# Performance work log

Measured on AMD Instinct MI355X. Metric: run time of the kernel, lower is better.

## Reference

```python
import jax, jax.numpy as jnp
import numpy as np

N = 100000   # vertices
T = 128      # temporal depth
E = 1600000  # edges (avg degree 16)
K = 9        # conv kernel size
PAD = 4      # 'same' padding -> T preserved
L = 3        # number of layers


def setup_inputs() -> dict:
    key = jax.random.key(0)
    ks = jax.random.split(key, 6)
    x = jax.random.normal(ks[0], (N, T), dtype=jnp.float32)
    edge_index = jax.random.randint(ks[1], (2, E), 0, N, dtype=jnp.int32)
    conv_w = jax.random.normal(ks[2], (L, 1, 1, K), dtype=jnp.float32) * (1.0 / np.sqrt(K))
    conv_b = jax.random.normal(ks[3], (L, 1), dtype=jnp.float32) * 0.1
    W_out = jax.random.normal(ks[4], (3, N), dtype=jnp.float32) * (1.0 / np.sqrt(N))
    b_out = jax.random.normal(ks[5], (3,), dtype=jnp.float32) * 0.1
    return {"x": x, "edge_index": edge_index, "conv_w": conv_w,
            "conv_b": conv_b, "W_out": W_out, "b_out": b_out}


def _conv1d(x, w, b):
    # x: [N, T], w: [1, 1, K] (OIH), b: [1]; torch Conv1d = cross-correlation.
    y = jax.lax.conv_general_dilated(
        x[:, None, :], w, window_strides=(1,), padding=[(PAD, PAD)],
        dimension_numbers=("NCH", "OIH", "NCH"))
    return y[:, 0, :] + b  # [N, T]


def reference(x, edge_index, conv_w, conv_b, W_out, b_out):
    # add_self_loops: append (i, i) for every node
    loop = jnp.arange(N, dtype=edge_index.dtype)
    src = jnp.concatenate([edge_index[0], loop])  # message sources
    dst = jnp.concatenate([edge_index[1], loop])  # aggregation targets
    # in-degree counts (>=1 due to self loops) for mean aggregation
    cnt = jax.ops.segment_sum(jnp.ones(src.shape, jnp.float32), dst,
                              num_segments=N)[:, None]  # [N, 1]
    for i in range(L):
        h = _conv1d(x, conv_w[i], conv_b[i])                    # [N, T]
        s = jax.ops.segment_sum(h[src], dst, num_segments=N)    # scatter-sum of gathered msgs
        x = jax.nn.relu(s / cnt)                                # mean aggr + relu
    x = x.reshape(-1, N)            # [T, N] (row-major view like torch .view)
    return x @ W_out.T + b_out      # [T, 3]
```

## Files before the change

kernel.cpp:

```cpp
#include <hip/hip_runtime.h>

#define NN 100000
#define TT 128
#define EE 1600000
#define KK 9
#define NSPLIT 16

#define BSH 9
#define BMASK 511
#define NBUCK 196
#define BCAP 10240
#define EPB 4096
#define BINB 391
#define CVTB 3125

typedef _Float16 f16;
typedef __attribute__((ext_vector_type(2))) _Float16 f16x2;
typedef __attribute__((ext_vector_type(4))) _Float16 f16x4;
typedef __attribute__((ext_vector_type(8))) _Float16 f16x8;

union HU8 { f16x8 h; int4 i; };

__global__ __launch_bounds__(1024)
void bin_cvt_kernel(const int* __restrict__ ei, int* __restrict__ gcursor,
                    unsigned int* __restrict__ binned,
                    const float4* __restrict__ x, f16x4* __restrict__ x16,
                    float* __restrict__ out) {
    __shared__ int hist[NBUCK];
    __shared__ int gbase[NBUCK];
    int tid = threadIdx.x;

    if (blockIdx.x >= BINB + CVTB) {
        if (tid < TT * 3) out[tid] = 0.0f;
        return;
    }
    if (blockIdx.x >= BINB) {
        int i = (blockIdx.x - BINB) * 1024 + tid;
        float4 v = x[i];
        f16x4 o;
        o.x = (f16)v.x; o.y = (f16)v.y; o.z = (f16)v.z; o.w = (f16)v.w;
        x16[i] = o;
        return;
    }

    if (tid < NBUCK) hist[tid] = 0;
    __syncthreads();
    int base = blockIdx.x * EPB;
    unsigned int val[4];
    short bkt[4];
    short rank[4];
#pragma unroll
    for (int k = 0; k < 4; k++) {
        int e = base + k * 1024 + tid;
        bkt[k] = -1;
        if (e < EE) {
            int s = ei[e];
            int d = ei[EE + e];
            bkt[k] = (short)(d >> BSH);
            val[k] = ((unsigned int)(d & BMASK) << 20) | (unsigned int)s;
            rank[k] = (short)atomicAdd(&hist[bkt[k]], 1);
        }
    }
    __syncthreads();
    if (tid < NBUCK) gbase[tid] = hist[tid] ? atomicAdd(&gcursor[tid], hist[tid]) : 0;
    __syncthreads();
#pragma unroll
    for (int k = 0; k < 4; k++) {
        if (bkt[k] >= 0)
            binned[(size_t)bkt[k] * BCAP + gbase[bkt[k]] + (int)rank[k]] = val[k];
    }
}

__global__ __launch_bounds__(1024)
void bucket_csr_kernel(const unsigned int* __restrict__ binned,
                       const int* __restrict__ gcursor,
                       int* __restrict__ offsets,
                       float* __restrict__ inv_cnt,
                       int* __restrict__ col) {
    __shared__ int hist[512];
    __shared__ int cur[512];
    __shared__ int smB[256];
    __shared__ int sc[512];
    int b = blockIdx.x;
    int tid = threadIdx.x;

    if (tid < 256) smB[tid] = (tid < NBUCK) ? gcursor[tid] : 0;
    __syncthreads();
    for (int off = 1; off < 256; off <<= 1) {
        int v = 0;
        if (tid < 256 && tid >= off) v = smB[tid - off];
        __syncthreads();
        if (tid < 256) smB[tid] += v;
        __syncthreads();
    }
    int bucket_base = (b == 0) ? 0 : smB[b - 1];
    if (b == 0 && tid == 0) offsets[NN] = EE;

    int cnt = gcursor[b];
    const unsigned int* ePtr = binned + (size_t)b * BCAP;
    if (tid < 512) hist[tid] = 0;
    __syncthreads();
    for (int j = tid; j < cnt; j += 1024)
        atomicAdd(&hist[ePtr[j] >> 20], 1);
    __syncthreads();
    int d = (tid < 512) ? hist[tid] : 0;
    if (tid < 512) sc[tid] = d;
    __syncthreads();
    for (int off = 1; off < 512; off <<= 1) {
        int v = 0;
        if (tid < 512 && tid >= off) v = sc[tid - off];
        __syncthreads();
        if (tid < 512) sc[tid] += v;
        __syncthreads();
    }
    if (tid < 512) {
        int node = (b << BSH) + tid;
        int pos = bucket_base + sc[tid] - d;
        if (node < NN) {
            offsets[node] = pos;
            inv_cnt[node] = 1.0f / (1.0f + (float)d);
            cur[tid] = pos;
        }
    }
    __syncthreads();
    for (int j = tid; j < cnt; j += 1024) {
        unsigned int v = ePtr[j];
        int pos = atomicAdd(&cur[v >> 20], 1);
        col[pos] = (int)(v & 0xFFFFF);
    }
}

__global__ __launch_bounds__(256)
void fused_layer_kernel(const f16x8* __restrict__ xin,
                        const int* __restrict__ offsets,
                        const int* __restrict__ col,
                        const float* __restrict__ inv_cnt,
                        const float* __restrict__ w9,
                        const float* __restrict__ bptr,
                        f16x8* __restrict__ yout) {
    __shared__ __align__(16) f16 sb[4][144];
    int tid = threadIdx.x;
    int lane = tid & 63;
    int q = lane >> 4;
    int p = lane & 15;
    int w = tid >> 6;
    int node = __builtin_amdgcn_readfirstlane(blockIdx.x * 4 + w);

    float wr[KK];
#pragma unroll
    for (int k = 0; k < KK; k++) wr[k] = w9[k];
    float bb = bptr[0];

    if (tid < 32) {
        int n = tid >> 3, k = tid & 7;
        ((int*)&sb[n][0])[(k < 4) ? k : (64 + k)] = 0;
    }

    int lo = offsets[node], hi = offsets[node + 1];
    int cnt = hi - lo;
    int my_col = (lane < cnt) ? col[lo + lane] : 0;
    int jn = cnt < 64 ? cnt : 64;

    const f16 z = (f16)0;
    f16x8 acc0 = {z, z, z, z, z, z, z, z};
    f16x8 acc1 = {z, z, z, z, z, z, z, z};
    if (q == 0) acc0 = xin[(node << 4) | p];

    int j = 0;
    for (; j + 7 < jn; j += 8) {
        int c0 = __shfl(my_col, j + q);
        int c1 = __shfl(my_col, j + 4 + q);
        f16x8 v0 = xin[(c0 << 4) | p];
        f16x8 v1 = xin[(c1 << 4) | p];
        acc0 += v0;
        acc1 += v1;
    }
    for (; j + 3 < jn; j += 4) {
        int c = __shfl(my_col, j + q);
        acc0 += xin[(c << 4) | p];
    }
    if (j < jn) {
        int rem = jn - j;
        int c = __shfl(my_col, j + (q < rem ? q : 0));
        f16x8 v = xin[(c << 4) | p];
        if (q < rem) acc1 += v;
    }
    for (int k = 64; k < cnt; k++) {
        int c = col[lo + k];
        f16x8 v = xin[(c << 4) | p];
        if (q == 0) acc0 += v;
    }
    acc0 += acc1;

    {
        HU8 u; u.h = acc0;
        int4 o;
        o.x = __shfl_xor(u.i.x, 16); o.y = __shfl_xor(u.i.y, 16);
        o.z = __shfl_xor(u.i.z, 16); o.w = __shfl_xor(u.i.w, 16);
        HU8 w2; w2.i = o;
        acc0 += w2.h;
        u.h = acc0;
        o.x = __shfl_xor(u.i.x, 32); o.y = __shfl_xor(u.i.y, 32);
        o.z = __shfl_xor(u.i.z, 32); o.w = __shfl_xor(u.i.w, 32);
        w2.i = o;
        acc0 += w2.h;
    }

    if (q == 0) *(f16x8*)&sb[w][8 + p * 8] = acc0;
    __syncthreads();

    int t0 = (tid & 63) * 2;
    float A[10];
    const f16x2* sp = (const f16x2*)&sb[w][4 + t0];
#pragma unroll
    for (int i = 0; i < 5; i++) {
        f16x2 v = sp[i];
        A[2 * i]     = (float)v.x;
        A[2 * i + 1] = (float)v.y;
    }
    float ic = inv_cnt[node];
    float r0 = 0.0f, r1 = 0.0f;
#pragma unroll
    for (int k = 0; k < KK; k++) {
        r0 += wr[k] * A[k];
        r1 += wr[k] * A[k + 1];
    }
    r0 = fmaxf(r0 * ic + bb, 0.0f);
    r1 = fmaxf(r1 * ic + bb, 0.0f);
    f16x2 o;
    o.x = (f16)r0;
    o.y = (f16)r1;
    ((f16x2*)yout)[node * 64 + (t0 >> 1)] = o;
}

__global__ void out_kernel(const f16* __restrict__ y3, const float* __restrict__ Wout,
                           const float* __restrict__ bout, float* __restrict__ out) {
    int t = blockIdx.x;
    int sp = blockIdx.y;
    int tid = threadIdx.x;
    const int per = NN / NSPLIT;
    int lo = sp * per;
    int hi = lo + per;
    float a0 = 0.0f, a1 = 0.0f, a2 = 0.0f;
    for (int n = lo + tid * 2; n < hi; n += 512) {
        f16x2 v2 = *(const f16x2*)(y3 + (size_t)t * NN + n);
        float vx = (float)v2.x, vy = (float)v2.y;
        float2 wA = *(const float2*)(Wout + n);
        float2 wB = *(const float2*)(Wout + NN + n);
        float2 wC = *(const float2*)(Wout + 2 * NN + n);
        a0 += vx * wA.x + vy * wA.y;
        a1 += vx * wB.x + vy * wB.y;
        a2 += vx * wC.x + vy * wC.y;
    }
    for (int o = 32; o > 0; o >>= 1) {
        a0 += __shfl_down(a0, o);
        a1 += __shfl_down(a1, o);
        a2 += __shfl_down(a2, o);
    }
    __shared__ float red[4][3];
    int wave = tid >> 6;
    if ((tid & 63) == 0) {
        red[wave][0] = a0;
        red[wave][1] = a1;
        red[wave][2] = a2;
    }
    __syncthreads();
    if (tid == 0) {
        float r0 = red[0][0] + red[1][0] + red[2][0] + red[3][0];
        float r1 = red[0][1] + red[1][1] + red[2][1] + red[3][1];
        float r2 = red[0][2] + red[1][2] + red[2][2] + red[3][2];
        if (sp == 0) {
            r0 += bout[0];
            r1 += bout[1];
            r2 += bout[2];
        }
        atomicAdd(&out[t * 3 + 0], r0);
        atomicAdd(&out[t * 3 + 1], r1);
        atomicAdd(&out[t * 3 + 2], r2);
    }
}

extern "C" void kernel_launch(void* const* d_in, const int* in_sizes, int n_in,
                              void* d_out, int out_size, void* d_ws, size_t ws_size,
                              hipStream_t stream) {
    const float4* x    = (const float4*)d_in[0];
    const int*    ei   = (const int*)d_in[1];
    const float*  cw   = (const float*)d_in[2];
    const float*  cb   = (const float*)d_in[3];
    const float*  Wout = (const float*)d_in[4];
    const float*  bout = (const float*)d_in[5];
    float* out = (float*)d_out;

    char* ws = (char*)d_ws;
    size_t off = 0;
    auto alloc = [&](size_t bytes) -> void* {
        void* p = ws + off;
        off += (bytes + 255) & ~(size_t)255;
        return p;
    };
    f16x8*        x16     = (f16x8*)alloc((size_t)NN * TT * 2);
    f16x8*        yA      = (f16x8*)alloc((size_t)NN * TT * 2);
    f16x8*        yB      = (f16x8*)alloc((size_t)NN * TT * 2);
    unsigned int* binned  = (unsigned int*)alloc((size_t)NBUCK * BCAP * 4);
    int*          gcursor = (int*)alloc((size_t)NBUCK * 4);
    int*          offsets = (int*)alloc((size_t)(NN + 1) * 4);
    float*        inv_cnt = (float*)alloc((size_t)NN * 4);
    int*          col     = (int*)alloc((size_t)EE * 4);

    hipMemsetAsync(gcursor, 0, (size_t)NBUCK * 4, stream);
    bin_cvt_kernel<<<BINB + CVTB + 1, 1024, 0, stream>>>(ei, gcursor, binned,
                                                         x, (f16x4*)x16, out);
    bucket_csr_kernel<<<NBUCK, 1024, 0, stream>>>(binned, gcursor, offsets, inv_cnt, col);

    fused_layer_kernel<<<NN / 4, 256, 0, stream>>>(x16, offsets, col, inv_cnt,
                                                   cw + 0 * KK, cb + 0, yA);
    fused_layer_kernel<<<NN / 4, 256, 0, stream>>>(yA, offsets, col, inv_cnt,
                                                   cw + 1 * KK, cb + 1, yB);
    fused_layer_kernel<<<NN / 4, 256, 0, stream>>>(yB, offsets, col, inv_cnt,
                                                   cw + 2 * KK, cb + 2, yA);

    out_kernel<<<dim3(TT, NSPLIT), 256, 0, stream>>>((const f16*)yA, Wout, bout, out);
}
```

Before: 326.5 us.

## Split conv from aggregation, half-row gather per block with XCD-aware node mapping

Result: slower. 372.8 us (+14.2%).

```diff
diff --git a/kernel.cpp b/kernel.cpp
--- a/kernel.cpp
+++ b/kernel.cpp
@@ -5,6 +5,7 @@
 #define EE 1600000
 #define KK 9
 #define NSPLIT 16
+#define ZROW NN
 
 #define BSH 9
 #define BMASK 511
@@ -12,7 +13,7 @@
 #define BCAP 10240
 #define EPB 4096
 #define BINB 391
-#define CVTB 3125
+#define CONVB 6250
 
 typedef _Float16 f16;
 typedef __attribute__((ext_vector_type(2))) _Float16 f16x2;
@@ -24,22 +25,45 @@
 __global__ __launch_bounds__(1024)
 void bin_cvt_kernel(const int* __restrict__ ei, int* __restrict__ gcursor,
                     unsigned int* __restrict__ binned,
-                    const float4* __restrict__ x, f16x4* __restrict__ x16,
-                    float* __restrict__ out) {
+                    const float2* __restrict__ x, f16x2* __restrict__ C1,
+                    const float* __restrict__ w9, float* __restrict__ out,
+                    int* __restrict__ zx, int* __restrict__ zy, int* __restrict__ zz) {
     __shared__ int hist[NBUCK];
     __shared__ int gbase[NBUCK];
-    int tid = threadIdx.x;
-
-    if (blockIdx.x >= BINB + CVTB) {
+    __shared__ float As[16][136];
+    int tid = threadIdx.x;
+
+    if (blockIdx.x >= BINB + CONVB) {
         if (tid < TT * 3) out[tid] = 0.0f;
+        int k = tid - 512;
+        if (k >= 0 && k < 64)         zx[k]       = 0;
+        else if (k >= 64 && k < 128)  zy[k - 64]  = 0;
+        else if (k >= 128 && k < 192) zz[k - 128] = 0;
         return;
     }
     if (blockIdx.x >= BINB) {
-        int i = (blockIdx.x - BINB) * 1024 + tid;
-        float4 v = x[i];
-        f16x4 o;
-        o.x = (f16)v.x; o.y = (f16)v.y; o.z = (f16)v.z; o.w = (f16)v.w;
-        x16[i] = o;
+        int w = tid >> 6, lane = tid & 63;
+        int row = (blockIdx.x - BINB) * 16 + w;
+        float wr[KK];
+#pragma unroll
+        for (int k = 0; k < KK; k++) wr[k] = w9[k];
+        float2 v = x[row * 64 + lane];
+        *(float2*)&As[w][4 + 2 * lane] = v;
+        if (lane < 4) { As[w][lane] = 0.0f; As[w][132 + lane] = 0.0f; }
+        float Awin[10];
+#pragma unroll
+        for (int i = 0; i < 5; i++) {
+            float2 t = *(float2*)&As[w][2 * lane + 2 * i];
+            Awin[2 * i] = t.x; Awin[2 * i + 1] = t.y;
+        }
+        float r0 = 0.0f, r1 = 0.0f;
+#pragma unroll
+        for (int k = 0; k < KK; k++) {
+            r0 += wr[k] * Awin[k];
+            r1 += wr[k] * Awin[k + 1];
+        }
+        f16x2 o; o.x = (f16)r0; o.y = (f16)r1;
+        C1[row * 64 + lane] = o;
         return;
     }
 
@@ -69,6 +93,36 @@
         if (bkt[k] >= 0)
             binned[(size_t)bkt[k] * BCAP + gbase[bkt[k]] + (int)rank[k]] = val[k];
     }
+}
+
+__global__ __launch_bounds__(1024)
+void conv_kernel(const f16x2* __restrict__ yin, const float* __restrict__ w9,
+                 f16x2* __restrict__ C) {
+    __shared__ float As[16][136];
+    int tid = threadIdx.x;
+    int w = tid >> 6, lane = tid & 63;
+    int row = blockIdx.x * 16 + w;
+    float wr[KK];
+#pragma unroll
+    for (int k = 0; k < KK; k++) wr[k] = w9[k];
+    f16x2 v = yin[row * 64 + lane];
+    As[w][4 + 2 * lane] = (float)v.x;
+    As[w][5 + 2 * lane] = (float)v.y;
+    if (lane < 4) { As[w][lane] = 0.0f; As[w][132 + lane] = 0.0f; }
+    float Awin[10];
+#pragma unroll
+    for (int i = 0; i < 5; i++) {
+        float2 t = *(float2*)&As[w][2 * lane + 2 * i];
+        Awin[2 * i] = t.x; Awin[2 * i + 1] = t.y;
+    }
+    float r0 = 0.0f, r1 = 0.0f;
+#pragma unroll
+    for (int k = 0; k < KK; k++) {
+        r0 += wr[k] * Awin[k];
+        r1 += wr[k] * Awin[k + 1];
+    }
+    f16x2 o; o.x = (f16)r0; o.y = (f16)r1;
+    C[row * 64 + lane] = o;
 }
 
 __global__ __launch_bounds__(1024)
@@ -131,73 +185,85 @@
 }
 
 __global__ __launch_bounds__(256)
-void fused_layer_kernel(const f16x8* __restrict__ xin,
+void fused_layer_kernel(const f16x8* __restrict__ C,
                         const int* __restrict__ offsets,
                         const int* __restrict__ col,
                         const float* __restrict__ inv_cnt,
-                        const float* __restrict__ w9,
                         const float* __restrict__ bptr,
                         f16x8* __restrict__ yout) {
-    __shared__ __align__(16) f16 sb[4][144];
     int tid = threadIdx.x;
     int lane = tid & 63;
-    int q = lane >> 4;
-    int p = lane & 15;
+    int g = lane >> 3;
+    int p = lane & 7;
     int w = tid >> 6;
-    int node = __builtin_amdgcn_readfirstlane(blockIdx.x * 4 + w);
-
-    float wr[KK];
-#pragma unroll
-    for (int k = 0; k < KK; k++) wr[k] = w9[k];
-    float bb = bptr[0];
-
-    if (tid < 32) {
-        int n = tid >> 3, k = tid & 7;
-        ((int*)&sb[n][0])[(k < 4) ? k : (64 + k)] = 0;
-    }
+    unsigned int bid = blockIdx.x;
+    int xcd  = bid & 7;
+    int half = xcd >> 2;
+    int quad = (int)(bid >> 3) * 4 + (bid & 3);
+    int node = __builtin_amdgcn_readfirstlane(quad * 4 + w);
+    int base = half * 8 + p;
 
     int lo = offsets[node], hi = offsets[node + 1];
     int cnt = hi - lo;
-    int my_col = (lane < cnt) ? col[lo + lane] : 0;
+    int my_col = (lane < cnt) ? col[lo + lane] : ZROW;
     int jn = cnt < 64 ? cnt : 64;
 
     const f16 z = (f16)0;
     f16x8 acc0 = {z, z, z, z, z, z, z, z};
     f16x8 acc1 = {z, z, z, z, z, z, z, z};
-    if (q == 0) acc0 = xin[(node << 4) | p];
-
-    int j = 0;
-    for (; j + 7 < jn; j += 8) {
-        int c0 = __shfl(my_col, j + q);
-        int c1 = __shfl(my_col, j + 4 + q);
-        f16x8 v0 = xin[(c0 << 4) | p];
-        f16x8 v1 = xin[(c1 << 4) | p];
-        acc0 += v0;
-        acc1 += v1;
-    }
-    for (; j + 3 < jn; j += 4) {
-        int c = __shfl(my_col, j + q);
-        acc0 += xin[(c << 4) | p];
-    }
-    if (j < jn) {
-        int rem = jn - j;
-        int c = __shfl(my_col, j + (q < rem ? q : 0));
-        f16x8 v = xin[(c << 4) | p];
-        if (q < rem) acc1 += v;
+    if (g == 0) acc0 = C[(node << 4) + base];
+
+    if (jn <= 32) {
+        int c0 = __shfl(my_col, g);
+        int c1 = __shfl(my_col, 8 + g);
+        int c2 = __shfl(my_col, 16 + g);
+        int c3 = __shfl(my_col, 24 + g);
+        f16x8 u0 = C[(c0 << 4) + base];
+        f16x8 u1 = C[(c1 << 4) + base];
+        f16x8 u2 = C[(c2 << 4) + base];
+        f16x8 u3 = C[(c3 << 4) + base];
+        acc0 += u0; acc1 += u1;
+        acc0 += u2; acc1 += u3;
+    } else {
+        int c0 = __shfl(my_col, g);
+        int c1 = __shfl(my_col, 8 + g);
+        int c2 = __shfl(my_col, 16 + g);
+        int c3 = __shfl(my_col, 24 + g);
+        int c4 = __shfl(my_col, 32 + g);
+        int c5 = __shfl(my_col, 40 + g);
+        int c6 = __shfl(my_col, 48 + g);
+        int c7 = __shfl(my_col, 56 + g);
+        f16x8 u0 = C[(c0 << 4) + base];
+        f16x8 u1 = C[(c1 << 4) + base];
+        f16x8 u2 = C[(c2 << 4) + base];
+        f16x8 u3 = C[(c3 << 4) + base];
+        f16x8 u4 = C[(c4 << 4) + base];
+        f16x8 u5 = C[(c5 << 4) + base];
+        f16x8 u6 = C[(c6 << 4) + base];
+        f16x8 u7 = C[(c7 << 4) + base];
+        acc0 += u0; acc1 += u1;
+        acc0 += u2; acc1 += u3;
+        acc0 += u4; acc1 += u5;
+        acc0 += u6; acc1 += u7;
     }
     for (int k = 64; k < cnt; k++) {
         int c = col[lo + k];
-        f16x8 v = xin[(c << 4) | p];
-        if (q == 0) acc0 += v;
+        f16x8 v = C[(c << 4) + base];
+        if (g == 0) acc0 += v;
     }
     acc0 += acc1;
 
     {
         HU8 u; u.h = acc0;
         int4 o;
+        o.x = __shfl_xor(u.i.x, 8);  o.y = __shfl_xor(u.i.y, 8);
+        o.z = __shfl_xor(u.i.z, 8);  o.w = __shfl_xor(u.i.w, 8);
+        HU8 w2; w2.i = o;
+        acc0 += w2.h;
+        u.h = acc0;
         o.x = __shfl_xor(u.i.x, 16); o.y = __shfl_xor(u.i.y, 16);
         o.z = __shfl_xor(u.i.z, 16); o.w = __shfl_xor(u.i.w, 16);
-        HU8 w2; w2.i = o;
+        w2.i = o;
         acc0 += w2.h;
         u.h = acc0;
         o.x = __shfl_xor(u.i.x, 32); o.y = __shfl_xor(u.i.y, 32);
@@ -206,31 +272,17 @@
         acc0 += w2.h;
     }
 
-    if (q == 0) *(f16x8*)&sb[w][8 + p * 8] = acc0;
-    __syncthreads();
-
-    int t0 = (tid & 63) * 2;
-    float A[10];
-    const f16x2* sp = (const f16x2*)&sb[w][4 + t0];
-#pragma unroll
-    for (int i = 0; i < 5; i++) {
-        f16x2 v = sp[i];
-        A[2 * i]     = (float)v.x;
-        A[2 * i + 1] = (float)v.y;
-    }
     float ic = inv_cnt[node];
-    float r0 = 0.0f, r1 = 0.0f;
-#pragma unroll
-    for (int k = 0; k < KK; k++) {
-        r0 += wr[k] * A[k];
-        r1 += wr[k] * A[k + 1];
-    }
-    r0 = fmaxf(r0 * ic + bb, 0.0f);
-    r1 = fmaxf(r1 * ic + bb, 0.0f);
-    f16x2 o;
-    o.x = (f16)r0;
-    o.y = (f16)r1;
-    ((f16x2*)yout)[node * 64 + (t0 >> 1)] = o;
+    float bb = bptr[0];
+    if (g == 0) {
+        f16x8 o;
+#pragma unroll
+        for (int i = 0; i < 8; i++) {
+            float t = fmaxf((float)acc0[i] * ic + bb, 0.0f);
+            o[i] = (f16)t;
+        }
+        yout[(node << 4) + base] = o;
+    }
 }
 
 __global__ void out_kernel(const f16* __restrict__ y3, const float* __restrict__ Wout,
@@ -283,7 +335,7 @@
 extern "C" void kernel_launch(void* const* d_in, const int* in_sizes, int n_in,
                               void* d_out, int out_size, void* d_ws, size_t ws_size,
                               hipStream_t stream) {
-    const float4* x    = (const float4*)d_in[0];
+    const float2* x    = (const float2*)d_in[0];
     const int*    ei   = (const int*)d_in[1];
     const float*  cw   = (const float*)d_in[2];
     const float*  cb   = (const float*)d_in[3];
@@ -298,9 +350,9 @@
         off += (bytes + 255) & ~(size_t)255;
         return p;
     };
-    f16x8*        x16     = (f16x8*)alloc((size_t)NN * TT * 2);
-    f16x8*        yA      = (f16x8*)alloc((size_t)NN * TT * 2);
-    f16x8*        yB      = (f16x8*)alloc((size_t)NN * TT * 2);
+    f16x8*        bufX    = (f16x8*)alloc((size_t)(NN + 1) * TT * 2);
+    f16x8*        bufY    = (f16x8*)alloc((size_t)(NN + 1) * TT * 2);
+    f16x8*        bufZ    = (f16x8*)alloc((size_t)(NN + 1) * TT * 2);
     unsigned int* binned  = (unsigned int*)alloc((size_t)NBUCK * BCAP * 4);
     int*          gcursor = (int*)alloc((size_t)NBUCK * 4);
     int*          offsets = (int*)alloc((size_t)(NN + 1) * 4);
@@ -308,16 +360,22 @@
     int*          col     = (int*)alloc((size_t)EE * 4);
 
     hipMemsetAsync(gcursor, 0, (size_t)NBUCK * 4, stream);
-    bin_cvt_kernel<<<BINB + CVTB + 1, 1024, 0, stream>>>(ei, gcursor, binned,
-                                                         x, (f16x4*)x16, out);
+    bin_cvt_kernel<<<BINB + CONVB + 1, 1024, 0, stream>>>(
+        ei, gcursor, binned, x, (f16x2*)bufX, cw + 0 * KK, out,
+        (int*)(bufX + (size_t)NN * 16), (int*)(bufY + (size_t)NN * 16),
+        (int*)(bufZ + (size_t)NN * 16));
     bucket_csr_kernel<<<NBUCK, 1024, 0, stream>>>(binned, gcursor, offsets, inv_cnt, col);
 
-    fused_layer_kernel<<<NN / 4, 256, 0, stream>>>(x16, offsets, col, inv_cnt,
-                                                   cw + 0 * KK, cb + 0, yA);
-    fused_layer_kernel<<<NN / 4, 256, 0, stream>>>(yA, offsets, col, inv_cnt,
-                                                   cw + 1 * KK, cb + 1, yB);
-    fused_layer_kernel<<<NN / 4, 256, 0, stream>>>(yB, offsets, col, inv_cnt,
-                                                   cw + 2 * KK, cb + 2, yA);
-
-    out_kernel<<<dim3(TT, NSPLIT), 256, 0, stream>>>((const f16*)yA, Wout, bout, out);
-}
+    fused_layer_kernel<<<50000, 256, 0, stream>>>(bufX, offsets, col, inv_cnt,
+                                                  cb + 0, bufY);
+    conv_kernel<<<CONVB, 1024, 0, stream>>>((const f16x2*)bufY, cw + 1 * KK,
+                                            (f16x2*)bufZ);
+    fused_layer_kernel<<<50000, 256, 0, stream>>>(bufZ, offsets, col, inv_cnt,
+                                                  cb + 1, bufX);
+    conv_kernel<<<CONVB, 1024, 0, stream>>>((const f16x2*)bufX, cw + 2 * KK,
+                                            (f16x2*)bufY);
+    fused_layer_kernel<<<50000, 256, 0, stream>>>(bufY, offsets, col, inv_cnt,
+                                                  cb + 2, bufZ);
+
+    out_kernel<<<dim3(TT, NSPLIT), 256, 0, stream>>>((const f16*)bufZ, Wout, bout, out);
+}
```
